# Kernel tuning notes

Hardware: AMD Instinct MI355X
Metric: run time of the kernel (lower is better)

Reference implementation:

```python
import jax, jax.numpy as jnp
import numpy as np

N, E = 50000, 800000
DN, DE, H = 128, 64, 8
C = DN // H  # per-head dim = 16


def setup_inputs() -> dict:
    key = jax.random.key(0)
    ks = jax.random.split(key, 16)
    s = 0.05
    inp = {
        "node_state": jax.random.normal(ks[0], (N, DN), jnp.float32),
        "edge_index": jax.random.randint(ks[1], (2, E), 0, N, jnp.int64 if jax.config.jax_enable_x64 else jnp.int32),
        "edge_state": jax.random.normal(ks[2], (E, DE), jnp.float32),
        # edge_proj: Linear(DE, DE)
        "W_edge": jax.random.normal(ks[3], (DE, DE), jnp.float32) * s,
        "b_edge": jnp.zeros((DE,), jnp.float32),
        # TransformerConv linears (in, out) layout: y = x @ W + b
        "Wq": jax.random.normal(ks[4], (DN, DN), jnp.float32) * s,
        "bq": jnp.zeros((DN,), jnp.float32),
        "Wk": jax.random.normal(ks[5], (DN, DN), jnp.float32) * s,
        "bk": jnp.zeros((DN,), jnp.float32),
        "Wv": jax.random.normal(ks[6], (DN, DN), jnp.float32) * s,
        "bv": jnp.zeros((DN,), jnp.float32),
        "We": jax.random.normal(ks[7], (DE, DN), jnp.float32) * s,  # lin_edge, no bias
        "Wskip": jax.random.normal(ks[8], (DN, DN), jnp.float32) * s,
        "bskip": jnp.zeros((DN,), jnp.float32),
        "Wbeta": jax.random.normal(ks[9], (3 * DN, 1), jnp.float32) * s,  # lin_beta, no bias
        "ln_g": jnp.ones((DN,), jnp.float32),
        "ln_b": jnp.zeros((DN,), jnp.float32),
    }
    return inp


def reference(node_state, edge_index, edge_state, W_edge, b_edge, Wq, bq, Wk, bk,
              Wv, bv, We, Wskip, bskip, Wbeta, ln_g, ln_b):
    n = node_state.shape[0]
    src, dst = edge_index[0], edge_index[1]

    # edge_proj
    edge_attr = edge_state @ W_edge + b_edge  # [E, DE]

    # TransformerConv (beta=True, concat=True, dropout in eval mode)
    q = (node_state @ Wq + bq).reshape(n, H, C)
    k = (node_state @ Wk + bk).reshape(n, H, C)
    v = (node_state @ Wv + bv).reshape(n, H, C)
    e = (edge_attr @ We).reshape(-1, H, C)  # [E, H, C]

    kj = k[src] + e                                        # [E, H, C]
    alpha = jnp.sum(q[dst] * kj, axis=-1) / np.sqrt(C)     # [E, H]

    # segment softmax over destination nodes
    amax = jax.ops.segment_max(alpha, dst, num_segments=n)  # [N, H]
    ex = jnp.exp(alpha - amax[dst])
    denom = jax.ops.segment_sum(ex, dst, num_segments=n)    # [N, H]
    a = ex / denom[dst]                                     # [E, H]

    msg = (v[src] + e) * a[:, :, None]                      # [E, H, C]
    out = jax.ops.segment_sum(msg, dst, num_segments=n).reshape(n, DN)

    # beta-gated skip
    x_r = node_state @ Wskip + bskip
    beta = jax.nn.sigmoid(jnp.concatenate([out, x_r, out - x_r], axis=-1) @ Wbeta)  # [N, 1]
    out = beta * x_r + (1.0 - beta) * out

    # LayerNorm
    mu = jnp.mean(out, axis=-1, keepdims=True)
    var = jnp.mean(jnp.square(out - mu), axis=-1, keepdims=True)
    normed = (out - mu) * jax.lax.rsqrt(var + 1e-5) * ln_g + ln_b

    # residual + relu (dropout is identity in eval)
    return node_state + jax.nn.relu(normed)
```

## Files before the change

### kernel.cpp

```cpp
#include <hip/hip_runtime.h>
#include <cstdint>
#include <cstddef>

#define NN 50000
#define NE 800000

typedef short bf16x8 __attribute__((ext_vector_type(8)));
typedef float f32x4 __attribute__((ext_vector_type(4)));
typedef float f32x2 __attribute__((ext_vector_type(2)));

__device__ __forceinline__ float b2f(unsigned short s) {
  union { unsigned int u; float f; } x; x.u = ((unsigned int)s) << 16; return x.f;
}
__device__ __forceinline__ unsigned short f2b(float f) {
  union { float f; unsigned int u; } x; x.f = f;
  unsigned int r = x.u + 0x7FFFu + ((x.u >> 16) & 1u);
  return (unsigned short)(r >> 16);
}

#define WS_WCE    0u
#define WS_BCE    16384u
#define WS_WCEF   20480u
#define WS_WALLF  40960u
#define WS_BALL   172032u
#define WS_QB     180224u
#define WS_KB     12980224u
#define WS_VB     25780224u
#define WS_XR     38580224u
#define WS_EB     64180224u
#define WS_CNT    268980224u
#define WS_OFF    269180224u
#define WS_CUR    269380224u
#define WS_BSUM   269580224u
#define WS_POS    269584320u
#define WS_SRCS   272784320u

__global__ void k_prep(const float* __restrict__ W_edge, const float* __restrict__ b_edge,
                       const float* __restrict__ We, unsigned short* __restrict__ wce,
                       float* __restrict__ bce) {
  int i = blockIdx.x;
  int j = threadIdx.x;
  float s = 0.f;
  for (int m = 0; m < 64; ++m) s += W_edge[i*64+m] * We[m*128+j];
  wce[i*128+j] = f2b(s);
  if (i == 0) {
    float bb = 0.f;
    for (int m = 0; m < 64; ++m) bb += b_edge[m] * We[m*128+j];
    bce[j] = bb;
  }
}

__global__ void k_pack_wce(const unsigned short* __restrict__ wce, unsigned short* __restrict__ wcef) {
  int fb = blockIdx.x;
  int ct = fb >> 1, s = fb & 1;
  int l = threadIdx.x;
  unsigned short* dst = wcef + (((size_t)(ct*2+s))*64 + l)*8;
  int col = ct*16 + (l & 15);
  int k0 = s*32 + (l >> 4)*8;
  #pragma unroll
  for (int j = 0; j < 8; ++j) dst[j] = wce[(k0+j)*128 + col];
}

__global__ void k_pack_wall(const float* __restrict__ Wq, const float* __restrict__ Wk,
                            const float* __restrict__ Wv, const float* __restrict__ Ws,
                            unsigned short* __restrict__ wallf) {
  int fb = blockIdx.x;
  int mat = fb >> 5, ct = (fb >> 2) & 7, s = fb & 3;
  int l = threadIdx.x;
  const float* W = (mat==0) ? Wq : (mat==1) ? Wk : (mat==2) ? Wv : Ws;
  unsigned short* dst = wallf + ((((size_t)(mat*8+ct))*4 + s)*64 + l)*8;
  int col = ct*16 + (l & 15);
  int k0 = s*32 + (l >> 4)*8;
  #pragma unroll
  for (int j = 0; j < 8; ++j) dst[j] = f2b(W[(k0+j)*128 + col]);
}

__global__ void k_pack_bias(const float* __restrict__ bq, const float* __restrict__ bk,
                            const float* __restrict__ bv, const float* __restrict__ bs,
                            float* __restrict__ ball) {
  int m = blockIdx.x, c = threadIdx.x;
  const float* b = (m==0) ? bq : (m==1) ? bk : (m==2) ? bv : bs;
  ball[m*128 + c] = b[c];
}

__global__ void __launch_bounds__(256) k_mfma_all(
    const float* __restrict__ x, const unsigned short* __restrict__ wallf,
    const float* __restrict__ ball,
    unsigned short* __restrict__ qb, unsigned char* __restrict__ kb,
    unsigned char* __restrict__ vb, float* __restrict__ xr,
    const float* __restrict__ es, const unsigned short* __restrict__ wcef,
    const float* __restrict__ bce, const int* __restrict__ pos,
    unsigned char* __restrict__ eb) {
  __shared__ char smem[18432];
  int b = blockIdx.x;
  int l = threadIdx.x & 63, w = threadIdx.x >> 6;
  int g = l >> 4, ln = l & 15;

  if (b % 5 == 0) {
    int tile = b / 5;
    if (tile >= ((NN + 63)/64) * 4) return;
    int mat = tile & 3;
    int n0 = (tile >> 2) * 64;
    unsigned short* sA = (unsigned short*)smem;
    for (int i = 0; i < 4; ++i) {
      int c = threadIdx.x + i*256;
      int row = c >> 4, ch = c & 15;
      int sw = (ch & 8) | ((ch & 7) ^ (row & 7));
      unsigned short tmp[8];
      if (n0 + row < NN) {
        const float* src = x + (size_t)(n0+row)*128 + ch*8;
        float4 f0 = *(const float4*)src;
        float4 f1 = *(const float4*)(src + 4);
        tmp[0]=f2b(f0.x); tmp[1]=f2b(f0.y); tmp[2]=f2b(f0.z); tmp[3]=f2b(f0.w);
        tmp[4]=f2b(f1.x); tmp[5]=f2b(f1.y); tmp[6]=f2b(f1.z); tmp[7]=f2b(f1.w);
      } else {
        #pragma unroll
        for (int j = 0; j < 8; ++j) tmp[j] = 0;
      }
      *(uint4*)&sA[row*128 + sw*8] = *(const uint4*)tmp;
    }
    __syncthreads();
    f32x4 acc[8];
    #pragma unroll
    for (int ct = 0; ct < 8; ++ct) acc[ct] = (f32x4){0.f,0.f,0.f,0.f};
    int row = w*16 + ln;
    for (int s = 0; s < 4; ++s) {
      int ch = s*4 + g;
      int sw = (ch & 8) | ((ch & 7) ^ (row & 7));
      bf16x8 bfr = *(const bf16x8*)&sA[row*128 + sw*8];
      #pragma unroll
      for (int ct = 0; ct < 8; ++ct) {
        bf16x8 wf = *(const bf16x8*)(wallf + ((((size_t)(mat*8+ct))*4 + s)*64 + l)*8);
        acc[ct] = __builtin_amdgcn_mfma_f32_16x16x32_bf16(wf, bfr, acc[ct], 0, 0, 0);
      }
    }
    int node = n0 + row;
    if (node >= NN) return;
    #pragma unroll
    for (int ct = 0; ct < 8; ++ct) {
      int c0 = ct*16 + g*4;
      float4 bi = *(const float4*)(ball + mat*128 + c0);
      float v0 = acc[ct][0] + bi.x, v1 = acc[ct][1] + bi.y;
      float v2 = acc[ct][2] + bi.z, v3 = acc[ct][3] + bi.w;
      if (mat == 3) {
        float4 o = {v0, v1, v2, v3};
        *(float4*)(xr + (size_t)node*128 + c0) = o;
      } else if (mat == 0) {
        unsigned short o[4] = {f2b(v0), f2b(v1), f2b(v2), f2b(v3)};
        *(uint2*)(qb + (size_t)node*128 + c0) = *(const uint2*)o;
      } else {
        int pk = 0;
        pk = __builtin_amdgcn_cvt_pk_fp8_f32(v0, v1, pk, false);
        pk = __builtin_amdgcn_cvt_pk_fp8_f32(v2, v3, pk, true);
        unsigned char* dst = (mat==1) ? kb : vb;
        *(int*)(dst + (size_t)node*128 + c0) = pk;
      }
    }
  } else {
    int tile = b - b/5 - 1;
    if (tile >= NE/64) return;
    int e0 = tile * 64;
    unsigned short* sA = (unsigned short*)smem;
    unsigned char*  sO8 = (unsigned char*)(smem + 8192);
    for (int i = 0; i < 2; ++i) {
      int c = threadIdx.x + i*256;
      int row = c >> 3, ch = c & 7;
      int sw = ch ^ (row & 7);
      const float* src = es + (size_t)(e0+row)*64 + ch*8;
      float4 f0 = *(const float4*)src;
      float4 f1 = *(const float4*)(src + 4);
      unsigned short tmp[8];
      tmp[0]=f2b(f0.x); tmp[1]=f2b(f0.y); tmp[2]=f2b(f0.z); tmp[3]=f2b(f0.w);
      tmp[4]=f2b(f1.x); tmp[5]=f2b(f1.y); tmp[6]=f2b(f1.z); tmp[7]=f2b(f1.w);
      *(uint4*)&sA[row*64 + sw*8] = *(const uint4*)tmp;
    }
    __syncthreads();
    f32x4 acc[8];
    #pragma unroll
    for (int ct = 0; ct < 8; ++ct) acc[ct] = (f32x4){0.f,0.f,0.f,0.f};
    int row = w*16 + ln;
    #pragma unroll
    for (int s = 0; s < 2; ++s) {
      int ch = (s*4 + g) ^ (row & 7);
      bf16x8 bfr = *(const bf16x8*)&sA[row*64 + ch*8];
      #pragma unroll
      for (int ct = 0; ct < 8; ++ct) {
        bf16x8 wf = *(const bf16x8*)(wcef + (((size_t)(ct*2+s))*64 + l)*8);
        acc[ct] = __builtin_amdgcn_mfma_f32_16x16x32_bf16(wf, bfr, acc[ct], 0, 0, 0);
      }
    }
    #pragma unroll
    for (int ct = 0; ct < 8; ++ct) {
      int c0 = ct*16 + g*4;
      float4 bi = *(const float4*)(bce + c0);
      int pk = 0;
      pk = __builtin_amdgcn_cvt_pk_fp8_f32(acc[ct][0]+bi.x, acc[ct][1]+bi.y, pk, false);
      pk = __builtin_amdgcn_cvt_pk_fp8_f32(acc[ct][2]+bi.z, acc[ct][3]+bi.w, pk, true);
      int ch = ct ^ (row & 7);
      *(int*)&sO8[row*160 + ch*16 + g*4] = pk;
    }
    __syncthreads();
    int rrow = threadIdx.x >> 3;
    int rch  = threadIdx.x & 7;
    #pragma unroll
    for (int it = 0; it < 2; ++it) {
      int r = it*32 + rrow;
      int swc = rch ^ (r & 7);
      uint4 val = *(const uint4*)&sO8[r*160 + swc*16];
      int prow = pos[e0 + r];
      *(uint4*)(eb + (size_t)prow*128 + rch*16) = val;
    }
  }
}

__global__ void __launch_bounds__(256) k_hist(const int* __restrict__ ei, int* __restrict__ cnt) {
  int t = blockIdx.x * 256 + threadIdx.x;
  if (t < NE) atomicAdd(&cnt[ei[NE + t]], 1);
}

__global__ void __launch_bounds__(256) k_scanA(const int* __restrict__ cnt,
    int* __restrict__ off, int* __restrict__ bsum) {
  __shared__ int s[256];
  int i = blockIdx.x * 256 + threadIdx.x;
  int v = (i < NN) ? cnt[i] : 0;
  s[threadIdx.x] = v;
  __syncthreads();
  #pragma unroll
  for (int d = 1; d < 256; d <<= 1) {
    int t = (threadIdx.x >= d) ? s[threadIdx.x - d] : 0;
    __syncthreads();
    s[threadIdx.x] += t;
    __syncthreads();
  }
  if (i < NN) off[i] = s[threadIdx.x] - v;
  if (threadIdx.x == 255) bsum[blockIdx.x] = s[255];
}

__global__ void __launch_bounds__(256) k_scanB(int* __restrict__ bsum, int nb) {
  __shared__ int s[256];
  int v = (threadIdx.x < nb) ? bsum[threadIdx.x] : 0;
  s[threadIdx.x] = v;
  __syncthreads();
  #pragma unroll
  for (int d = 1; d < 256; d <<= 1) {
    int t = (threadIdx.x >= d) ? s[threadIdx.x - d] : 0;
    __syncthreads();
    s[threadIdx.x] += t;
    __syncthreads();
  }
  if (threadIdx.x < nb) bsum[threadIdx.x] = s[threadIdx.x] - v;
}

__global__ void __launch_bounds__(256) k_scanC(int* __restrict__ off,
    const int* __restrict__ bsum, int* __restrict__ cur) {
  int i = blockIdx.x * 256 + threadIdx.x;
  if (i < NN) {
    int o = off[i] + bsum[blockIdx.x];
    off[i] = o;
    cur[i] = o;
  }
}

__global__ void __launch_bounds__(256) k_scatter(const int* __restrict__ ei,
    int* __restrict__ cur, int* __restrict__ pos, int* __restrict__ srcs) {
  int t = blockIdx.x * 256 + threadIdx.x;
  if (t < NE) {
    int d = ei[NE + t];
    int p = atomicAdd(&cur[d], 1);
    pos[t] = p;
    srcs[p] = ei[t];
  }
}

__global__ void __launch_bounds__(256) k_attn(
    const int* __restrict__ off, const int* __restrict__ cnt,
    const int* __restrict__ srcs,
    const unsigned short* __restrict__ qb, const unsigned char* __restrict__ kb,
    const unsigned char* __restrict__ vb, const unsigned char* __restrict__ eb,
    const float* __restrict__ xr, const float* __restrict__ x,
    const float* __restrict__ Wb, const float* __restrict__ ln_g,
    const float* __restrict__ ln_b, float* __restrict__ out) {
  int wid = threadIdx.x >> 6, lane = threadIdx.x & 63;
  int n = blockIdx.x * 4 + wid;
  if (n >= NN) return;
  int c = lane * 2;

  unsigned int qu = *(const unsigned int*)(qb + (size_t)n*128 + c);
  float q0 = b2f((unsigned short)(qu & 0xffffu)), q1 = b2f((unsigned short)(qu >> 16));

  int start = off[n], m = cnt[n];
  const int* sp = srcs + start;
  const unsigned char* ep = eb + (size_t)start*128 + c;
  float acc0 = 0.f, acc1 = 0.f, den = 0.f;

  auto body = [&](unsigned int ku2, unsigned int eu2, unsigned int vu2) {
    f32x2 ef = __builtin_amdgcn_cvt_pk_f32_fp8((int)eu2, false);
    f32x2 kf = __builtin_amdgcn_cvt_pk_f32_fp8((int)ku2, false);
    f32x2 vf = __builtin_amdgcn_cvt_pk_f32_fp8((int)vu2, false);
    float p = q0*(kf[0] + ef[0]) + q1*(kf[1] + ef[1]);
    p += __shfl_xor(p, 1);
    p += __shfl_xor(p, 2);
    p += __shfl_xor(p, 4);
    float a = __expf(p * 0.25f);
    den  += a;
    acc0 += a * (vf[0] + ef[0]);
    acc1 += a * (vf[1] + ef[1]);
  };

  int i = 0;
  for (; i + 4 <= m; i += 4) {
    int sA = sp[i], sB = sp[i+1], sC = sp[i+2], sD = sp[i+3];
    unsigned int euA = *(const unsigned short*)(ep + (size_t)(i+0)*128);
    unsigned int euB = *(const unsigned short*)(ep + (size_t)(i+1)*128);
    unsigned int euC = *(const unsigned short*)(ep + (size_t)(i+2)*128);
    unsigned int euD = *(const unsigned short*)(ep + (size_t)(i+3)*128);
    unsigned int kuA = *(const unsigned short*)(kb + (size_t)sA*128 + c);
    unsigned int vuA = *(const unsigned short*)(vb + (size_t)sA*128 + c);
    unsigned int kuB = *(const unsigned short*)(kb + (size_t)sB*128 + c);
    unsigned int vuB = *(const unsigned short*)(vb + (size_t)sB*128 + c);
    unsigned int kuC = *(const unsigned short*)(kb + (size_t)sC*128 + c);
    unsigned int vuC = *(const unsigned short*)(vb + (size_t)sC*128 + c);
    unsigned int kuD = *(const unsigned short*)(kb + (size_t)sD*128 + c);
    unsigned int vuD = *(const unsigned short*)(vb + (size_t)sD*128 + c);
    body(kuA, euA, vuA);
    body(kuB, euB, vuB);
    body(kuC, euC, vuC);
    body(kuD, euD, vuD);
  }
  for (; i < m; ++i) {
    int sA = sp[i];
    unsigned int euA = *(const unsigned short*)(ep + (size_t)i*128);
    unsigned int kuA = *(const unsigned short*)(kb + (size_t)sA*128 + c);
    unsigned int vuA = *(const unsigned short*)(vb + (size_t)sA*128 + c);
    body(kuA, euA, vuA);
  }

  float inv = (m > 0) ? 1.f / den : 0.f;
  float o0 = acc0 * inv, o1 = acc1 * inv;

  float2 r = *(const float2*)(xr + (size_t)n*128 + c);
  float p = o0*Wb[c] + o1*Wb[c+1] + r.x*Wb[128+c] + r.y*Wb[128+c+1]
          + (o0-r.x)*Wb[256+c] + (o1-r.y)*Wb[256+c+1];
  #pragma unroll
  for (int offs = 32; offs > 0; offs >>= 1) p += __shfl_xor(p, offs);
  float beta = 1.f / (1.f + __expf(-p));
  float g0 = beta*r.x + (1.f-beta)*o0;
  float g1 = beta*r.y + (1.f-beta)*o1;
  float msum = g0 + g1;
  #pragma unroll
  for (int offs = 32; offs > 0; offs >>= 1) msum += __shfl_xor(msum, offs);
  msum *= (1.f/128.f);
  float d0 = g0 - msum, d1 = g1 - msum;
  float vv = d0*d0 + d1*d1;
  #pragma unroll
  for (int offs = 32; offs > 0; offs >>= 1) vv += __shfl_xor(vv, offs);
  vv *= (1.f/128.f);
  float rs = rsqrtf(vv + 1e-5f);
  float n0 = d0*rs*ln_g[c]   + ln_b[c];
  float n1 = d1*rs*ln_g[c+1] + ln_b[c+1];
  float2 xv = *(const float2*)(x + (size_t)n*128 + c);
  float2 res;
  res.x = xv.x + fmaxf(n0, 0.f);
  res.y = xv.y + fmaxf(n1, 0.f);
  *(float2*)(out + (size_t)n*128 + c) = res;
}

extern "C" void kernel_launch(void* const* d_in, const int* in_sizes, int n_in,
                              void* d_out, int out_size, void* d_ws, size_t ws_size,
                              hipStream_t stream) {
  const float* node   = (const float*)d_in[0];
  const int*   ei     = (const int*)  d_in[1];
  const float* es     = (const float*)d_in[2];
  const float* W_edge = (const float*)d_in[3];
  const float* b_edge = (const float*)d_in[4];
  const float* Wq     = (const float*)d_in[5];
  const float* bq     = (const float*)d_in[6];
  const float* Wk     = (const float*)d_in[7];
  const float* bk     = (const float*)d_in[8];
  const float* Wv     = (const float*)d_in[9];
  const float* bv     = (const float*)d_in[10];
  const float* We     = (const float*)d_in[11];
  const float* Wskip  = (const float*)d_in[12];
  const float* bskip  = (const float*)d_in[13];
  const float* Wbeta  = (const float*)d_in[14];
  const float* ln_g   = (const float*)d_in[15];
  const float* ln_b   = (const float*)d_in[16];

  char* ws = (char*)d_ws;
  unsigned short* wce   = (unsigned short*)(ws + WS_WCE);
  float*          bce   = (float*)(ws + WS_BCE);
  unsigned short* wcef  = (unsigned short*)(ws + WS_WCEF);
  unsigned short* wallf = (unsigned short*)(ws + WS_WALLF);
  float*          ball  = (float*)(ws + WS_BALL);
  unsigned short* qb  = (unsigned short*)(ws + WS_QB);
  unsigned char*  kb  = (unsigned char*)(ws + WS_KB);
  unsigned char*  vb  = (unsigned char*)(ws + WS_VB);
  float*          xr  = (float*)(ws + WS_XR);
  unsigned char*  eb  = (unsigned char*)(ws + WS_EB);
  int*            cnt = (int*)(ws + WS_CNT);
  int*            off = (int*)(ws + WS_OFF);
  int*            cur = (int*)(ws + WS_CUR);
  int*            bsm = (int*)(ws + WS_BSUM);
  int*            pos = (int*)(ws + WS_POS);
  int*            srcs= (int*)(ws + WS_SRCS);

  hipMemsetAsync(cnt, 0, (size_t)NN*4, stream);

  k_prep<<<64, 128, 0, stream>>>(W_edge, b_edge, We, wce, bce);
  k_pack_wce<<<16, 64, 0, stream>>>(wce, wcef);
  k_pack_wall<<<128, 64, 0, stream>>>(Wq, Wk, Wv, Wskip, wallf);
  k_pack_bias<<<4, 128, 0, stream>>>(bq, bk, bv, bskip, ball);

  const int nbScan = (NN + 255)/256;
  k_hist<<<(NE + 255)/256, 256, 0, stream>>>(ei, cnt);
  k_scanA<<<nbScan, 256, 0, stream>>>(cnt, off, bsm);
  k_scanB<<<1, 256, 0, stream>>>(bsm, nbScan);
  k_scanC<<<nbScan, 256, 0, stream>>>(off, bsm, cur);
  k_scatter<<<(NE + 255)/256, 256, 0, stream>>>(ei, cur, pos, srcs);

  const int nodeTiles = ((NN + 63)/64) * 4;
  const int grid = 5 * nodeTiles;
  k_mfma_all<<<grid, 256, 0, stream>>>(node, wallf, ball, qb, kb, vb, xr,
                                       es, wcef, bce, pos, eb);

  k_attn<<<(NN + 3)/4, 256, 0, stream>>>(off, cnt, srcs, qb, kb, vb, eb,
                                         xr, node, Wbeta, ln_g, ln_b, (float*)d_out);
}
```

Baseline: 284.4 us.

## Make projection kernel persistent with double-buffered edge prefetch; unroll attention gather by 8

Turns the fused node/edge projection kernel into a persistent kernel with a fixed grid. Node blocks loop over node tiles, and edge blocks loop over edge tiles, prefetching the next tile's edge_state rows and scatter positions into registers while the current tile runs its MFMAs. This is meant to hide global load latency and cut per-block launch and prologue overhead. The attention kernel also gains an 8-edge unrolled gather loop so more loads are in flight, at the cost of more registers and possibly lower occupancy.

```diff
diff --git a/kernel.cpp b/kernel.cpp
--- a/kernel.cpp
+++ b/kernel.cpp
@@ -4,6 +4,12 @@
 
 #define NN 50000
 #define NE 800000
+
+#define NODE_BLOCKS 680
+#define EDGE_BLOCKS 1368
+#define TOTAL_BLOCKS (NODE_BLOCKS + EDGE_BLOCKS)
+#define NET (NE/64)
+#define NNT (((NN+63)/64)*4)
 
 typedef short bf16x8 __attribute__((ext_vector_type(8)));
 typedef float f32x4 __attribute__((ext_vector_type(4)));
@@ -91,125 +97,152 @@
     const float* __restrict__ es, const unsigned short* __restrict__ wcef,
     const float* __restrict__ bce, const int* __restrict__ pos,
     unsigned char* __restrict__ eb) {
-  __shared__ char smem[18432];
-  int b = blockIdx.x;
+  __shared__ unsigned short sA[64*128];
+  __shared__ unsigned char  sO8[64*160];
   int l = threadIdx.x & 63, w = threadIdx.x >> 6;
   int g = l >> 4, ln = l & 15;
 
-  if (b % 5 == 0) {
-    int tile = b / 5;
-    if (tile >= ((NN + 63)/64) * 4) return;
-    int mat = tile & 3;
-    int n0 = (tile >> 2) * 64;
-    unsigned short* sA = (unsigned short*)smem;
-    for (int i = 0; i < 4; ++i) {
-      int c = threadIdx.x + i*256;
-      int row = c >> 4, ch = c & 15;
-      int sw = (ch & 8) | ((ch & 7) ^ (row & 7));
-      unsigned short tmp[8];
-      if (n0 + row < NN) {
-        const float* src = x + (size_t)(n0+row)*128 + ch*8;
-        float4 f0 = *(const float4*)src;
-        float4 f1 = *(const float4*)(src + 4);
-        tmp[0]=f2b(f0.x); tmp[1]=f2b(f0.y); tmp[2]=f2b(f0.z); tmp[3]=f2b(f0.w);
-        tmp[4]=f2b(f1.x); tmp[5]=f2b(f1.y); tmp[6]=f2b(f1.z); tmp[7]=f2b(f1.w);
-      } else {
+  if (blockIdx.x < NODE_BLOCKS) {
+    for (int tile = blockIdx.x; tile < NNT; tile += NODE_BLOCKS) {
+      int mat = tile & 3;
+      int n0 = (tile >> 2) * 64;
+      for (int i = 0; i < 4; ++i) {
+        int c = threadIdx.x + i*256;
+        int row = c >> 4, ch = c & 15;
+        int sw = (ch & 8) | ((ch & 7) ^ (row & 7));
+        unsigned short tmp[8];
+        if (n0 + row < NN) {
+          const float* src = x + (size_t)(n0+row)*128 + ch*8;
+          float4 f0 = *(const float4*)src;
+          float4 f1 = *(const float4*)(src + 4);
+          tmp[0]=f2b(f0.x); tmp[1]=f2b(f0.y); tmp[2]=f2b(f0.z); tmp[3]=f2b(f0.w);
+          tmp[4]=f2b(f1.x); tmp[5]=f2b(f1.y); tmp[6]=f2b(f1.z); tmp[7]=f2b(f1.w);
+        } else {
+          #pragma unroll
+          for (int j = 0; j < 8; ++j) tmp[j] = 0;
+        }
+        *(uint4*)&sA[row*128 + sw*8] = *(const uint4*)tmp;
+      }
+      __syncthreads();
+      f32x4 acc[8];
+      #pragma unroll
+      for (int ct = 0; ct < 8; ++ct) acc[ct] = (f32x4){0.f,0.f,0.f,0.f};
+      int row = w*16 + ln;
+      for (int s = 0; s < 4; ++s) {
+        int ch = s*4 + g;
+        int sw = (ch & 8) | ((ch & 7) ^ (row & 7));
+        bf16x8 bfr = *(const bf16x8*)&sA[row*128 + sw*8];
         #pragma unroll
-        for (int j = 0; j < 8; ++j) tmp[j] = 0;
+        for (int ct = 0; ct < 8; ++ct) {
+          bf16x8 wf = *(const bf16x8*)(wallf + ((((size_t)(mat*8+ct))*4 + s)*64 + l)*8);
+          acc[ct] = __builtin_amdgcn_mfma_f32_16x16x32_bf16(wf, bfr, acc[ct], 0, 0, 0);
+        }
       }
-      *(uint4*)&sA[row*128 + sw*8] = *(const uint4*)tmp;
+      int node = n0 + row;
+      if (node < NN) {
+        #pragma unroll
+        for (int ct = 0; ct < 8; ++ct) {
+          int c0 = ct*16 + g*4;
+          float4 bi = *(const float4*)(ball + mat*128 + c0);
+          float v0 = acc[ct][0] + bi.x, v1 = acc[ct][1] + bi.y;
+          float v2 = acc[ct][2] + bi.z, v3 = acc[ct][3] + bi.w;
+          if (mat == 3) {
+            float4 o = {v0, v1, v2, v3};
+            *(float4*)(xr + (size_t)node*128 + c0) = o;
+          } else if (mat == 0) {
+            unsigned short o[4] = {f2b(v0), f2b(v1), f2b(v2), f2b(v3)};
+            *(uint2*)(qb + (size_t)node*128 + c0) = *(const uint2*)o;
+          } else {
+            int pk = 0;
+            pk = __builtin_amdgcn_cvt_pk_fp8_f32(v0, v1, pk, false);
+            pk = __builtin_amdgcn_cvt_pk_fp8_f32(v2, v3, pk, true);
+            unsigned char* dst = (mat==1) ? kb : vb;
+            *(int*)(dst + (size_t)node*128 + c0) = pk;
+          }
+        }
+      }
+      __syncthreads();
     }
-    __syncthreads();
-    f32x4 acc[8];
-    #pragma unroll
-    for (int ct = 0; ct < 8; ++ct) acc[ct] = (f32x4){0.f,0.f,0.f,0.f};
-    int row = w*16 + ln;
-    for (int s = 0; s < 4; ++s) {
-      int ch = s*4 + g;
-      int sw = (ch & 8) | ((ch & 7) ^ (row & 7));
-      bf16x8 bfr = *(const bf16x8*)&sA[row*128 + sw*8];
-      #pragma unroll
-      for (int ct = 0; ct < 8; ++ct) {
-        bf16x8 wf = *(const bf16x8*)(wallf + ((((size_t)(mat*8+ct))*4 + s)*64 + l)*8);
-        acc[ct] = __builtin_amdgcn_mfma_f32_16x16x32_bf16(wf, bfr, acc[ct], 0, 0, 0);
+  } else {
+    int row = threadIdx.x >> 3, ch = threadIdx.x & 7;
+    float4 A0, A1, A2, A3; int Ap0 = 0, Ap1 = 0;
+    float4 B0, B1, B2, B3; int Bp0 = 0, Bp1 = 0;
+
+#define PFLOAD(T, a0, a1, a2, a3, p0, p1) do {                          \
+    int e0_ = (T)*64;                                                   \
+    const float* s0_ = es + (size_t)(e0_ + row)*64 + ch*8;              \
+    a0 = *(const float4*)s0_; a1 = *(const float4*)(s0_ + 4);           \
+    const float* s1_ = s0_ + 32*64;                                     \
+    a2 = *(const float4*)s1_; a3 = *(const float4*)(s1_ + 4);           \
+    p0 = pos[e0_ + row]; p1 = pos[e0_ + 32 + row];                      \
+  } while (0)
+
+#define ESTAGE(a0, a1, a2, a3) do {                                     \
+    unsigned short t_[8];                                               \
+    t_[0]=f2b(a0.x); t_[1]=f2b(a0.y); t_[2]=f2b(a0.z); t_[3]=f2b(a0.w); \
+    t_[4]=f2b(a1.x); t_[5]=f2b(a1.y); t_[6]=f2b(a1.z); t_[7]=f2b(a1.w); \
+    *(uint4*)&sA[row*64 + (ch^(row&7))*8] = *(const uint4*)t_;          \
+    t_[0]=f2b(a2.x); t_[1]=f2b(a2.y); t_[2]=f2b(a2.z); t_[3]=f2b(a2.w); \
+    t_[4]=f2b(a3.x); t_[5]=f2b(a3.y); t_[6]=f2b(a3.z); t_[7]=f2b(a3.w); \
+    int r2_ = row + 32;                                                 \
+    *(uint4*)&sA[r2_*64 + (ch^(r2_&7))*8] = *(const uint4*)t_;          \
+  } while (0)
+
+#define ECOMPUTE(p0, p1) do {                                           \
+    __syncthreads();                                                    \
+    f32x4 acc[8];                                                       \
+    _Pragma("unroll")                                                   \
+    for (int ct = 0; ct < 8; ++ct) acc[ct] = (f32x4){0.f,0.f,0.f,0.f};  \
+    int mrow_ = w*16 + ln;                                              \
+    _Pragma("unroll")                                                   \
+    for (int s = 0; s < 2; ++s) {                                       \
+      int ch_ = (s*4 + g) ^ (mrow_ & 7);                                \
+      bf16x8 bfr_ = *(const bf16x8*)&sA[mrow_*64 + ch_*8];              \
+      _Pragma("unroll")                                                 \
+      for (int ct = 0; ct < 8; ++ct) {                                  \
+        bf16x8 wf_ = *(const bf16x8*)(wcef + (((size_t)(ct*2+s))*64 + l)*8); \
+        acc[ct] = __builtin_amdgcn_mfma_f32_16x16x32_bf16(wf_, bfr_, acc[ct], 0, 0, 0); \
+      }                                                                 \
+    }                                                                   \
+    _Pragma("unroll")                                                   \
+    for (int ct = 0; ct < 8; ++ct) {                                    \
+      int c0_ = ct*16 + g*4;                                            \
+      float4 bi_ = *(const float4*)(bce + c0_);                         \
+      int pk_ = 0;                                                      \
+      pk_ = __builtin_amdgcn_cvt_pk_fp8_f32(acc[ct][0]+bi_.x, acc[ct][1]+bi_.y, pk_, false); \
+      pk_ = __builtin_amdgcn_cvt_pk_fp8_f32(acc[ct][2]+bi_.z, acc[ct][3]+bi_.w, pk_, true);  \
+      *(int*)&sO8[mrow_*160 + (ct^(mrow_&7))*16 + g*4] = pk_;           \
+    }                                                                   \
+    __syncthreads();                                                    \
+    {                                                                   \
+      uint4 v0_ = *(const uint4*)&sO8[row*160 + (ch^(row&7))*16];       \
+      *(uint4*)(eb + (size_t)(p0)*128 + ch*16) = v0_;                   \
+      int r2_ = row + 32;                                               \
+      uint4 v1_ = *(const uint4*)&sO8[r2_*160 + (ch^(r2_&7))*16];       \
+      *(uint4*)(eb + (size_t)(p1)*128 + ch*16) = v1_;                   \
+    }                                                                   \
+  } while (0)
+
+    int t = blockIdx.x - NODE_BLOCKS;
+    if (t < NET) {
+      PFLOAD(t, A0, A1, A2, A3, Ap0, Ap1);
+      while (true) {
+        int t2 = t + EDGE_BLOCKS;
+        ESTAGE(A0, A1, A2, A3);
+        if (t2 < NET) PFLOAD(t2, B0, B1, B2, B3, Bp0, Bp1);
+        ECOMPUTE(Ap0, Ap1);
+        if (t2 >= NET) break;
+        int t3 = t2 + EDGE_BLOCKS;
+        ESTAGE(B0, B1, B2, B3);
+        if (t3 < NET) PFLOAD(t3, A0, A1, A2, A3, Ap0, Ap1);
+        ECOMPUTE(Bp0, Bp1);
+        if (t3 >= NET) break;
+        t = t3;
       }
     }
-    int node = n0 + row;
-    if (node >= NN) return;
-    #pragma unroll
-    for (int ct = 0; ct < 8; ++ct) {
-      int c0 = ct*16 + g*4;
-      float4 bi = *(const float4*)(ball + mat*128 + c0);
-      float v0 = acc[ct][0] + bi.x, v1 = acc[ct][1] + bi.y;
-      float v2 = acc[ct][2] + bi.z, v3 = acc[ct][3] + bi.w;
-      if (mat == 3) {
-        float4 o = {v0, v1, v2, v3};
-        *(float4*)(xr + (size_t)node*128 + c0) = o;
-      } else if (mat == 0) {
-        unsigned short o[4] = {f2b(v0), f2b(v1), f2b(v2), f2b(v3)};
-        *(uint2*)(qb + (size_t)node*128 + c0) = *(const uint2*)o;
-      } else {
-        int pk = 0;
-        pk = __builtin_amdgcn_cvt_pk_fp8_f32(v0, v1, pk, false);
-        pk = __builtin_amdgcn_cvt_pk_fp8_f32(v2, v3, pk, true);
-        unsigned char* dst = (mat==1) ? kb : vb;
-        *(int*)(dst + (size_t)node*128 + c0) = pk;
-      }
-    }
-  } else {
-    int tile = b - b/5 - 1;
-    if (tile >= NE/64) return;
-    int e0 = tile * 64;
-    unsigned short* sA = (unsigned short*)smem;
-    unsigned char*  sO8 = (unsigned char*)(smem + 8192);
-    for (int i = 0; i < 2; ++i) {
-      int c = threadIdx.x + i*256;
-      int row = c >> 3, ch = c & 7;
-      int sw = ch ^ (row & 7);
-      const float* src = es + (size_t)(e0+row)*64 + ch*8;
-      float4 f0 = *(const float4*)src;
-      float4 f1 = *(const float4*)(src + 4);
-      unsigned short tmp[8];
-      tmp[0]=f2b(f0.x); tmp[1]=f2b(f0.y); tmp[2]=f2b(f0.z); tmp[3]=f2b(f0.w);
-      tmp[4]=f2b(f1.x); tmp[5]=f2b(f1.y); tmp[6]=f2b(f1.z); tmp[7]=f2b(f1.w);
-      *(uint4*)&sA[row*64 + sw*8] = *(const uint4*)tmp;
-    }
-    __syncthreads();
-    f32x4 acc[8];
-    #pragma unroll
-    for (int ct = 0; ct < 8; ++ct) acc[ct] = (f32x4){0.f,0.f,0.f,0.f};
-    int row = w*16 + ln;
-    #pragma unroll
-    for (int s = 0; s < 2; ++s) {
-      int ch = (s*4 + g) ^ (row & 7);
-      bf16x8 bfr = *(const bf16x8*)&sA[row*64 + ch*8];
-      #pragma unroll
-      for (int ct = 0; ct < 8; ++ct) {
-        bf16x8 wf = *(const bf16x8*)(wcef + (((size_t)(ct*2+s))*64 + l)*8);
-        acc[ct] = __builtin_amdgcn_mfma_f32_16x16x32_bf16(wf, bfr, acc[ct], 0, 0, 0);
-      }
-    }
-    #pragma unroll
-    for (int ct = 0; ct < 8; ++ct) {
-      int c0 = ct*16 + g*4;
-      float4 bi = *(const float4*)(bce + c0);
-      int pk = 0;
-      pk = __builtin_amdgcn_cvt_pk_fp8_f32(acc[ct][0]+bi.x, acc[ct][1]+bi.y, pk, false);
-      pk = __builtin_amdgcn_cvt_pk_fp8_f32(acc[ct][2]+bi.z, acc[ct][3]+bi.w, pk, true);
-      int ch = ct ^ (row & 7);
-      *(int*)&sO8[row*160 + ch*16 + g*4] = pk;
-    }
-    __syncthreads();
-    int rrow = threadIdx.x >> 3;
-    int rch  = threadIdx.x & 7;
-    #pragma unroll
-    for (int it = 0; it < 2; ++it) {
-      int r = it*32 + rrow;
-      int swc = rch ^ (r & 7);
-      uint4 val = *(const uint4*)&sO8[r*160 + swc*16];
-      int prow = pos[e0 + r];
-      *(uint4*)(eb + (size_t)prow*128 + rch*16) = val;
-    }
+#undef PFLOAD
+#undef ESTAGE
+#undef ECOMPUTE
   }
 }
 
@@ -308,24 +341,33 @@
   };
 
   int i = 0;
+  for (; i + 8 <= m; i += 8) {
+    int sn[8]; unsigned int eu[8], ku[8], vu[8];
+    #pragma unroll
+    for (int j = 0; j < 8; ++j) sn[j] = sp[i+j];
+    #pragma unroll
+    for (int j = 0; j < 8; ++j) eu[j] = *(const unsigned short*)(ep + (size_t)(i+j)*128);
+    #pragma unroll
+    for (int j = 0; j < 8; ++j) {
+      ku[j] = *(const unsigned short*)(kb + (size_t)sn[j]*128 + c);
+      vu[j] = *(const unsigned short*)(vb + (size_t)sn[j]*128 + c);
+    }
+    #pragma unroll
+    for (int j = 0; j < 8; ++j) body(ku[j], eu[j], vu[j]);
+  }
   for (; i + 4 <= m; i += 4) {
-    int sA = sp[i], sB = sp[i+1], sC = sp[i+2], sD = sp[i+3];
-    unsigned int euA = *(const unsigned short*)(ep + (size_t)(i+0)*128);
-    unsigned int euB = *(const unsigned short*)(ep + (size_t)(i+1)*128);
-    unsigned int euC = *(const unsigned short*)(ep + (size_t)(i+2)*128);
-    unsigned int euD = *(const unsigned short*)(ep + (size_t)(i+3)*128);
-    unsigned int kuA = *(const unsigned short*)(kb + (size_t)sA*128 + c);
-    unsigned int vuA = *(const unsigned short*)(vb + (size_t)sA*128 + c);
-    unsigned int kuB = *(const unsigned short*)(kb + (size_t)sB*128 + c);
-    unsigned int vuB = *(const unsigned short*)(vb + (size_t)sB*128 + c);
-    unsigned int kuC = *(const unsigned short*)(kb + (size_t)sC*128 + c);
-    unsigned int vuC = *(const unsigned short*)(vb + (size_t)sC*128 + c);
-    unsigned int kuD = *(const unsigned short*)(kb + (size_t)sD*128 + c);
-    unsigned int vuD = *(const unsigned short*)(vb + (size_t)sD*128 + c);
-    body(kuA, euA, vuA);
-    body(kuB, euB, vuB);
-    body(kuC, euC, vuC);
-    body(kuD, euD, vuD);
+    int sn[4]; unsigned int eu[4], ku[4], vu[4];
+    #pragma unroll
+    for (int j = 0; j < 4; ++j) sn[j] = sp[i+j];
+    #pragma unroll
+    for (int j = 0; j < 4; ++j) eu[j] = *(const unsigned short*)(ep + (size_t)(i+j)*128);
+    #pragma unroll
+    for (int j = 0; j < 4; ++j) {
+      ku[j] = *(const unsigned short*)(kb + (size_t)sn[j]*128 + c);
+      vu[j] = *(const unsigned short*)(vb + (size_t)sn[j]*128 + c);
+    }
+    #pragma unroll
+    for (int j = 0; j < 4; ++j) body(ku[j], eu[j], vu[j]);
   }
   for (; i < m; ++i) {
     int sA = sp[i];
@@ -418,10 +460,8 @@
   k_scanC<<<nbScan, 256, 0, stream>>>(off, bsm, cur);
   k_scatter<<<(NE + 255)/256, 256, 0, stream>>>(ei, cur, pos, srcs);
 
-  const int nodeTiles = ((NN + 63)/64) * 4;
-  const int grid = 5 * nodeTiles;
-  k_mfma_all<<<grid, 256, 0, stream>>>(node, wallf, ball, qb, kb, vb, xr,
-                                       es, wcef, bce, pos, eb);
+  k_mfma_all<<<TOTAL_BLOCKS, 256, 0, stream>>>(node, wallf, ball, qb, kb, vb, xr,
+                                               es, wcef, bce, pos, eb);
 
   k_attn<<<(NN + 3)/4, 256, 0, stream>>>(off, cnt, srcs, qb, kb, vb, eb,
                                          xr, node, Wbeta, ln_g, ln_b, (float*)d_out);
```

Result: slower. 309.8 us (+8.9%).

## Compute all four node projections per block and deepen gather unroll in attention

Applied to the files above, without the earlier changes.

Node-projection blocks now load and convert a 64-row node tile once and compute all four projections (q, k, v, skip) from it, rather than one projection per block. The grid interleave changes from 1-in-5 to 1-in-17 so node blocks are spread among edge blocks. Edge blocks prefetch their scatter positions into shared memory early. The attention kernel gets an 8-wide unrolled gather loop to keep more independent loads in flight, at the cost of more registers and longer-running node blocks.

```diff
diff --git a/kernel.cpp b/kernel.cpp
--- a/kernel.cpp
+++ b/kernel.cpp
@@ -4,6 +4,9 @@
 
 #define NN 50000
 #define NE 800000
+
+#define NNT ((NN + 63)/64)
+#define NET (NE/64)
 
 typedef short bf16x8 __attribute__((ext_vector_type(8)));
 typedef float f32x4 __attribute__((ext_vector_type(4)));
@@ -91,16 +94,15 @@
     const float* __restrict__ es, const unsigned short* __restrict__ wcef,
     const float* __restrict__ bce, const int* __restrict__ pos,
     unsigned char* __restrict__ eb) {
-  __shared__ char smem[18432];
+  __shared__ char smem[18688];
   int b = blockIdx.x;
   int l = threadIdx.x & 63, w = threadIdx.x >> 6;
   int g = l >> 4, ln = l & 15;
 
-  if (b % 5 == 0) {
-    int tile = b / 5;
-    if (tile >= ((NN + 63)/64) * 4) return;
-    int mat = tile & 3;
-    int n0 = (tile >> 2) * 64;
+  if (b % 17 == 0) {
+    int tile = b / 17;
+    if (tile >= NNT) return;
+    int n0 = tile * 64;
     unsigned short* sA = (unsigned short*)smem;
     for (int i = 0; i < 4; ++i) {
       int c = threadIdx.x + i*256;
@@ -120,48 +122,58 @@
       *(uint4*)&sA[row*128 + sw*8] = *(const uint4*)tmp;
     }
     __syncthreads();
-    f32x4 acc[8];
-    #pragma unroll
-    for (int ct = 0; ct < 8; ++ct) acc[ct] = (f32x4){0.f,0.f,0.f,0.f};
     int row = w*16 + ln;
+    int node = n0 + row;
+    bf16x8 bfr[4];
+    #pragma unroll
     for (int s = 0; s < 4; ++s) {
       int ch = s*4 + g;
       int sw = (ch & 8) | ((ch & 7) ^ (row & 7));
-      bf16x8 bfr = *(const bf16x8*)&sA[row*128 + sw*8];
+      bfr[s] = *(const bf16x8*)&sA[row*128 + sw*8];
+    }
+    for (int mat = 0; mat < 4; ++mat) {
+      f32x4 acc[8];
       #pragma unroll
-      for (int ct = 0; ct < 8; ++ct) {
-        bf16x8 wf = *(const bf16x8*)(wallf + ((((size_t)(mat*8+ct))*4 + s)*64 + l)*8);
-        acc[ct] = __builtin_amdgcn_mfma_f32_16x16x32_bf16(wf, bfr, acc[ct], 0, 0, 0);
+      for (int ct = 0; ct < 8; ++ct) acc[ct] = (f32x4){0.f,0.f,0.f,0.f};
+      #pragma unroll
+      for (int s = 0; s < 4; ++s) {
+        #pragma unroll
+        for (int ct = 0; ct < 8; ++ct) {
+          bf16x8 wf = *(const bf16x8*)(wallf + ((((size_t)(mat*8+ct))*4 + s)*64 + l)*8);
+          acc[ct] = __builtin_amdgcn_mfma_f32_16x16x32_bf16(wf, bfr[s], acc[ct], 0, 0, 0);
+        }
       }
-    }
-    int node = n0 + row;
-    if (node >= NN) return;
-    #pragma unroll
-    for (int ct = 0; ct < 8; ++ct) {
-      int c0 = ct*16 + g*4;
-      float4 bi = *(const float4*)(ball + mat*128 + c0);
-      float v0 = acc[ct][0] + bi.x, v1 = acc[ct][1] + bi.y;
-      float v2 = acc[ct][2] + bi.z, v3 = acc[ct][3] + bi.w;
-      if (mat == 3) {
-        float4 o = {v0, v1, v2, v3};
-        *(float4*)(xr + (size_t)node*128 + c0) = o;
-      } else if (mat == 0) {
-        unsigned short o[4] = {f2b(v0), f2b(v1), f2b(v2), f2b(v3)};
-        *(uint2*)(qb + (size_t)node*128 + c0) = *(const uint2*)o;
-      } else {
-        int pk = 0;
-        pk = __builtin_amdgcn_cvt_pk_fp8_f32(v0, v1, pk, false);
-        pk = __builtin_amdgcn_cvt_pk_fp8_f32(v2, v3, pk, true);
-        unsigned char* dst = (mat==1) ? kb : vb;
-        *(int*)(dst + (size_t)node*128 + c0) = pk;
+      if (node < NN) {
+        #pragma unroll
+        for (int ct = 0; ct < 8; ++ct) {
+          int c0 = ct*16 + g*4;
+          float4 bi = *(const float4*)(ball + mat*128 + c0);
+          float v0 = acc[ct][0] + bi.x, v1 = acc[ct][1] + bi.y;
+          float v2 = acc[ct][2] + bi.z, v3 = acc[ct][3] + bi.w;
+          if (mat == 3) {
+            float4 o = {v0, v1, v2, v3};
+            *(float4*)(xr + (size_t)node*128 + c0) = o;
+          } else if (mat == 0) {
+            unsigned short o[4] = {f2b(v0), f2b(v1), f2b(v2), f2b(v3)};
+            *(uint2*)(qb + (size_t)node*128 + c0) = *(const uint2*)o;
+          } else {
+            int pk = 0;
+            pk = __builtin_amdgcn_cvt_pk_fp8_f32(v0, v1, pk, false);
+            pk = __builtin_amdgcn_cvt_pk_fp8_f32(v2, v3, pk, true);
+            unsigned char* dst = (mat==1) ? kb : vb;
+            *(int*)(dst + (size_t)node*128 + c0) = pk;
+          }
+        }
       }
     }
   } else {
-    int tile = b - b/5 - 1;
-    if (tile >= NE/64) return;
+    int tile = b - b/17 - 1;
+    if (tile >= NET) return;
     int e0 = tile * 64;
-    unsigned short* sA = (unsigned short*)smem;
+    unsigned short* sA  = (unsigned short*)smem;
     unsigned char*  sO8 = (unsigned char*)(smem + 8192);
+    int*            sP  = (int*)(smem + 18432);
+    if (threadIdx.x < 64) sP[threadIdx.x] = pos[e0 + threadIdx.x];
     for (int i = 0; i < 2; ++i) {
       int c = threadIdx.x + i*256;
       int row = c >> 3, ch = c & 7;
@@ -207,7 +219,7 @@
       int r = it*32 + rrow;
       int swc = rch ^ (r & 7);
       uint4 val = *(const uint4*)&sO8[r*160 + swc*16];
-      int prow = pos[e0 + r];
+      int prow = sP[r];
       *(uint4*)(eb + (size_t)prow*128 + rch*16) = val;
     }
   }
@@ -308,24 +320,33 @@
   };
 
   int i = 0;
+  for (; i + 8 <= m; i += 8) {
+    int sn[8]; unsigned int eu[8], ku[8], vu[8];
+    #pragma unroll
+    for (int j = 0; j < 8; ++j) sn[j] = sp[i+j];
+    #pragma unroll
+    for (int j = 0; j < 8; ++j) eu[j] = *(const unsigned short*)(ep + (size_t)(i+j)*128);
+    #pragma unroll
+    for (int j = 0; j < 8; ++j) {
+      ku[j] = *(const unsigned short*)(kb + (size_t)sn[j]*128 + c);
+      vu[j] = *(const unsigned short*)(vb + (size_t)sn[j]*128 + c);
+    }
+    #pragma unroll
+    for (int j = 0; j < 8; ++j) body(ku[j], eu[j], vu[j]);
+  }
   for (; i + 4 <= m; i += 4) {
-    int sA = sp[i], sB = sp[i+1], sC = sp[i+2], sD = sp[i+3];
-    unsigned int euA = *(const unsigned short*)(ep + (size_t)(i+0)*128);
-    unsigned int euB = *(const unsigned short*)(ep + (size_t)(i+1)*128);
-    unsigned int euC = *(const unsigned short*)(ep + (size_t)(i+2)*128);
-    unsigned int euD = *(const unsigned short*)(ep + (size_t)(i+3)*128);
-    unsigned int kuA = *(const unsigned short*)(kb + (size_t)sA*128 + c);
-    unsigned int vuA = *(const unsigned short*)(vb + (size_t)sA*128 + c);
-    unsigned int kuB = *(const unsigned short*)(kb + (size_t)sB*128 + c);
-    unsigned int vuB = *(const unsigned short*)(vb + (size_t)sB*128 + c);
-    unsigned int kuC = *(const unsigned short*)(kb + (size_t)sC*128 + c);
-    unsigned int vuC = *(const unsigned short*)(vb + (size_t)sC*128 + c);
-    unsigned int kuD = *(const unsigned short*)(kb + (size_t)sD*128 + c);
-    unsigned int vuD = *(const unsigned short*)(vb + (size_t)sD*128 + c);
-    body(kuA, euA, vuA);
-    body(kuB, euB, vuB);
-    body(kuC, euC, vuC);
-    body(kuD, euD, vuD);
+    int sn[4]; unsigned int eu[4], ku[4], vu[4];
+    #pragma unroll
+    for (int j = 0; j < 4; ++j) sn[j] = sp[i+j];
+    #pragma unroll
+    for (int j = 0; j < 4; ++j) eu[j] = *(const unsigned short*)(ep + (size_t)(i+j)*128);
+    #pragma unroll
+    for (int j = 0; j < 4; ++j) {
+      ku[j] = *(const unsigned short*)(kb + (size_t)sn[j]*128 + c);
+      vu[j] = *(const unsigned short*)(vb + (size_t)sn[j]*128 + c);
+    }
+    #pragma unroll
+    for (int j = 0; j < 4; ++j) body(ku[j], eu[j], vu[j]);
   }
   for (; i < m; ++i) {
     int sA = sp[i];
@@ -418,8 +439,7 @@
   k_scanC<<<nbScan, 256, 0, stream>>>(off, bsm, cur);
   k_scatter<<<(NE + 255)/256, 256, 0, stream>>>(ei, cur, pos, srcs);
 
-  const int nodeTiles = ((NN + 63)/64) * 4;
-  const int grid = 5 * nodeTiles;
+  const int grid = 17 * NNT;
   k_mfma_all<<<grid, 256, 0, stream>>>(node, wallf, ball, qb, kb, vb, xr,
                                        es, wcef, bce, pos, eb);
 
```

After: 291.7 us. 1.03x slower.
